# Kernel optimization log

Measured on AMD Instinct MI355X. Metric: run time of the kernel, lower is better.

Reference implementation:

```python
import jax, jax.numpy as jnp
import numpy as np

N, E, F, CUTOFF = 50000, 500000, 64, 5.0
EPS_CN, EPS_LN = 1e-8, 1e-5


def _xavier(k, shape):
    lim = float(np.sqrt(6.0 / (shape[0] + shape[1])))
    return jax.random.uniform(k, shape, jnp.float32, -lim, lim)


def setup_inputs() -> dict:
    key = jax.random.key(0)
    ks = jax.random.split(key, 20)
    vn = jax.random.normal(ks[5], (E, 3), jnp.float32)
    vn = vn / jnp.linalg.norm(vn, axis=-1, keepdims=True)  # unit direction vectors
    return {
        "node_s": jax.random.normal(ks[0], (N, 1, F), jnp.float32),
        "node_v": jax.random.normal(ks[1], (N, 3, F), jnp.float32),
        "edge_s": jax.random.normal(ks[2], (E, 1, F), jnp.float32),
        "edge_v": jax.random.normal(ks[3], (E, 3, F), jnp.float32),
        "dist": jax.random.uniform(ks[4], (E, 1), jnp.float32) * CUTOFF,
        "vctr_norm": vn,
        "src": jax.random.randint(ks[6], (E,), 0, N),
        "dst": jax.random.randint(ks[7], (E,), 0, N),
        "W_nn": _xavier(ks[8], (2 * F, F)), "b_nn": jnp.zeros((F,), jnp.float32),
        "W_ep": _xavier(ks[9], (F, F)), "b_ep": jnp.zeros((F,), jnp.float32),
        "W_g1": _xavier(ks[10], (F, F)), "b_g1": jnp.zeros((F,), jnp.float32),
        "W_g2": _xavier(ks[11], (F, F)), "b_g2": jnp.zeros((F,), jnp.float32),
        "W_ev": _xavier(ks[12], (F, 3 * F)), "b_ev": jnp.zeros((3 * F,), jnp.float32),
        "W_nvout": _xavier(ks[13], (F, 3 * F)),
        "W_nvc": _xavier(ks[14], (2 * F, F)), "b_nvc": jnp.zeros((F,), jnp.float32),
        "W_nvp": _xavier(ks[15], (F, 2 * F)),
        "W_nsp": _xavier(ks[16], (F, 2 * F)), "b_nsp": jnp.zeros((2 * F,), jnp.float32),
        "ln_gamma": jnp.ones((F,), jnp.float32), "ln_beta": jnp.zeros((F,), jnp.float32),
        "cn_scale": jnp.ones((F,), jnp.float32),
    }


def reference(node_s, node_v, edge_s, edge_v, dist, vctr_norm, src, dst,
              W_nn, b_nn, W_ep, b_ep, W_g1, b_g1, W_g2, b_g2, W_ev, b_ev,
              W_nvout, W_nvc, b_nvc, W_nvp, W_nsp, b_nsp, ln_gamma, ln_beta, cn_scale):
    n_nodes = node_s.shape[0]
    # cosine cutoff [E,1]
    c = 0.5 * (jnp.cos(jnp.pi * dist / CUTOFF) + 1.0) * (dist < CUTOFF).astype(dist.dtype)
    # ---- edge scalar update (gather src/dst, small MLPs) ----
    nn_in = jnp.concatenate([node_s[src], node_s[dst]], axis=-1)        # [E,1,2F]
    node_neighbors = nn_in @ W_nn + b_nn                                # [E,1,F]
    edge_message = node_neighbors * (edge_s @ W_ep + b_ep)              # [E,1,F]
    h = jax.nn.silu(edge_message @ W_g1 + b_g1)                         # GateMLP hidden
    es_upd = (h @ W_g2 + b_g2) * c[..., None]                           # [E,1,F]
    # ---- edge vector update ----
    vch = es_upd @ W_ev + b_ev                                          # [E,1,3F]
    nch, ech, rch = jnp.split(vch, 3, axis=-1)
    ev_upd = node_v[src] * nch + edge_v * ech + vctr_norm[..., None] * rch  # [E,3,F]
    ev_upd = ev_upd * c[..., None]
    # ---- scatter-mean to destination nodes ----
    deg = jax.ops.segment_sum(jnp.ones((src.shape[0],), node_s.dtype), dst, num_segments=n_nodes)
    denom = jnp.maximum(deg, 1.0)[:, None, None]
    n_ev = jax.ops.segment_sum(ev_upd, dst, num_segments=n_nodes) / denom  # [N,3,F]
    n_es = jax.ops.segment_sum(es_upd, dst, num_segments=n_nodes) / denom  # [N,1,F]
    # ---- node vector update ----
    nv_o1, nv_o2, nv_o3 = jnp.split(n_ev @ W_nvout, 3, axis=-1)          # each [N,3,F]
    v_in = jnp.concatenate([n_es, jnp.linalg.norm(nv_o3, axis=1, keepdims=True)], axis=-1)  # [N,1,2F]
    v_channel = v_in @ W_nvc + b_nvc                                     # [N,1,F]
    nv_upd = nv_o1 * v_channel + nv_o2                                   # [N,3,F]
    # ---- node scalar update ----
    nvp1, nvp2 = jnp.split(nv_upd @ W_nvp, 2, axis=-1)                   # [N,3,F] each
    ns1, ns2 = jnp.split(jax.nn.silu(n_es @ W_nsp + b_nsp), 2, axis=-1)  # [N,1,F] each
    nv_dot = jnp.sum(nvp1 * nvp2, axis=1, keepdims=True)                 # [N,1,F]
    ns_upd = nv_dot * ns1 + ns2                                          # [N,1,F]
    # ---- residuals + norms ----
    node_s_out = ns_upd + node_s
    node_v_out = nv_upd + node_v
    edge_s_out = es_upd + edge_s
    edge_v_out = ev_upd + edge_v
    # CoorsNorm: normalize over the 3D axis, learnable per-channel scale
    vnorm = jnp.linalg.norm(node_v_out, axis=1, keepdims=True)
    node_v_out = node_v_out / jnp.maximum(vnorm, EPS_CN) * cn_scale
    # LayerNorm over feature dim
    mu = jnp.mean(node_s_out, axis=-1, keepdims=True)
    var = jnp.var(node_s_out, axis=-1, keepdims=True)
    node_s_out = (node_s_out - mu) / jnp.sqrt(var + EPS_LN) * ln_gamma + ln_beta
    return node_s_out, node_v_out, edge_s_out, edge_v_out
```

## Files before the change

kernel.cpp:

```cpp
#include <hip/hip_runtime.h>
#include <hip/hip_bf16.h>
#include <math.h>

typedef __attribute__((ext_vector_type(8))) short bf16x8;
typedef __attribute__((ext_vector_type(4))) float f32x4;

#define MFMA16(a, b, c) __builtin_amdgcn_mfma_f32_16x16x32_bf16((a), (b), (c), 0, 0, 0)

__device__ __forceinline__ float silu_f(float x) { return x / (1.0f + expf(-x)); }

__device__ __forceinline__ unsigned short f2bf(float f) {
  union { __hip_bfloat16 h; unsigned short u; } c;
  c.h = __float2bfloat16(f);
  return c.u;
}
__device__ __forceinline__ unsigned pk2(float a, float b) {
  return (unsigned)f2bf(a) | ((unsigned)f2bf(b) << 16);
}

__device__ __forceinline__ bf16x8 ld_act(const unsigned short* buf, int strideB, int ks, int lane) {
  int row = lane & 15;
  int off = row * strideB + ks * 64 + ((lane >> 4) << 4);
  off ^= (row & 7) << 4;
  return *(const bf16x8*)((const char*)buf + off);
}

__device__ __forceinline__ bf16x8 ld_w(const unsigned short* Wt, int rowbase, int strideB, int ks, int lane) {
  return *(const bf16x8*)((const char*)Wt + (size_t)(rowbase + (lane & 15)) * strideB + ks * 64 + ((lane >> 4) << 4));
}

__global__ void wprep_kernel(const float* __restrict__ W, unsigned short* __restrict__ Wt,
                             int K, int Nn) {
  int idx = blockIdx.x * 256 + threadIdx.x;
  if (idx < K * Nn) {
    int n = idx / K, k = idx - n * K;
    Wt[idx] = f2bf(W[(size_t)k * Nn + n]);
  }
}

__global__ void hist_kernel(const int* __restrict__ dst, int* __restrict__ cnt, int E) {
  int i = blockIdx.x * blockDim.x + threadIdx.x;
  if (i < E) atomicAdd(&cnt[dst[i]], 1);
}

__global__ __launch_bounds__(1024) void scan_kernel(int* __restrict__ cnt,
                                                    int* __restrict__ rowstart, int N) {
  __shared__ int wsum[16];
  const int tid = threadIdx.x;
  const int wv = tid >> 6;
  int carry = 0;
  for (int base = 0; base < N; base += 1024) {
    int i = base + tid;
    int v = (i < N) ? cnt[i] : 0;
    int x = v;
    #pragma unroll
    for (int o = 1; o < 64; o <<= 1) {
      int y = __shfl_up(x, o);
      if ((tid & 63) >= o) x += y;
    }
    if ((tid & 63) == 63) wsum[wv] = x;
    __syncthreads();
    if (tid < 16) {
      int s = wsum[tid];
      #pragma unroll
      for (int o = 1; o < 16; o <<= 1) {
        int y = __shfl_up(s, o);
        if (tid >= o) s += y;
      }
      wsum[tid] = s;
    }
    __syncthreads();
    int woff = (wv > 0) ? wsum[wv - 1] : 0;
    if (i < N) {
      int excl = carry + woff + x - v;
      rowstart[i] = excl;
      cnt[i] = excl;
    }
    carry += wsum[15];
    __syncthreads();
  }
  if (tid == 0) rowstart[N] = carry;
}

__global__ void scatter_kernel(const int* __restrict__ dst, int* __restrict__ cursor,
                               int* __restrict__ elist, int E) {
  int i = blockIdx.x * blockDim.x + threadIdx.x;
  if (i < E) {
    int pos = atomicAdd(&cursor[dst[i]], 1);
    elist[pos] = i;
  }
}

__global__ __launch_bounds__(256) void edge_kernel(
    const float* __restrict__ node_s, const float* __restrict__ node_v,
    const float* __restrict__ edge_s, const float* __restrict__ edge_v,
    const float* __restrict__ dist,   const float* __restrict__ vctr,
    const int* __restrict__ src,      const int* __restrict__ dst,
    const unsigned short* __restrict__ wnn_t, const float* __restrict__ b_nn,
    const unsigned short* __restrict__ wep_t, const float* __restrict__ b_ep,
    const unsigned short* __restrict__ wg1_t, const float* __restrict__ b_g1,
    const unsigned short* __restrict__ wg2_t, const float* __restrict__ b_g2,
    const unsigned short* __restrict__ wev_t, const float* __restrict__ b_ev,
    float* __restrict__ es_out, float* __restrict__ ev_out,
    int E, int n_tiles)
{
  __shared__ __align__(16) unsigned short lds[4 * 3072];
  const int wid  = threadIdx.x >> 6;
  const int lane = threadIdx.x & 63;
  const int tile = blockIdx.x * 4 + wid;
  if (tile >= n_tiles) return;
  const int ebase = tile * 16;
  unsigned short* bufA = lds + wid * 3072;
  unsigned short* bufB = bufA + 2048;

  const int m  = lane & 15;
  const int nb = lane >> 4;

  {
    const int sm = lane >> 5;
    const int kk = lane & 31;
    #pragma unroll
    for (int p = 0; p < 8; ++p) {
      int le = p * 2 + sm;
      int e = ebase + le; if (e >= E) e = E - 1;
      int s = src[e], d = dst[e];
      float2 vs = *(const float2*)(node_s + (size_t)s * 64 + 2 * kk);
      float2 vd = *(const float2*)(node_s + (size_t)d * 64 + 2 * kk);
      float2 ve = *(const float2*)(edge_s + (size_t)e * 64 + 2 * kk);
      unsigned swz = (le & 7) << 4;
      *(unsigned*)((char*)bufA + ((le * 256 + kk * 4) ^ swz))       = pk2(vs.x, vs.y);
      *(unsigned*)((char*)bufA + ((le * 256 + 128 + kk * 4) ^ swz)) = pk2(vd.x, vd.y);
      *(unsigned*)((char*)bufB + ((le * 128 + kk * 4) ^ swz))       = pk2(ve.x, ve.y);
    }
  }
  __builtin_amdgcn_wave_barrier();

  const f32x4 z4 = {0.0f, 0.0f, 0.0f, 0.0f};

  bf16x8 a0 = ld_act(bufA, 256, 0, lane), a1 = ld_act(bufA, 256, 1, lane);
  bf16x8 a2 = ld_act(bufA, 256, 2, lane), a3 = ld_act(bufA, 256, 3, lane);
  f32x4 accN[4] = {z4, z4, z4, z4};
  #pragma unroll
  for (int nt = 0; nt < 4; ++nt) {
    accN[nt] = MFMA16(ld_w(wnn_t, nt * 16, 256, 0, lane), a0, accN[nt]);
    accN[nt] = MFMA16(ld_w(wnn_t, nt * 16, 256, 1, lane), a1, accN[nt]);
    accN[nt] = MFMA16(ld_w(wnn_t, nt * 16, 256, 2, lane), a2, accN[nt]);
    accN[nt] = MFMA16(ld_w(wnn_t, nt * 16, 256, 3, lane), a3, accN[nt]);
  }

  bf16x8 b0 = ld_act(bufB, 128, 0, lane), b1 = ld_act(bufB, 128, 1, lane);
  f32x4 accP[4] = {z4, z4, z4, z4};
  #pragma unroll
  for (int nt = 0; nt < 4; ++nt) {
    accP[nt] = MFMA16(ld_w(wep_t, nt * 16, 128, 0, lane), b0, accP[nt]);
    accP[nt] = MFMA16(ld_w(wep_t, nt * 16, 128, 1, lane), b1, accP[nt]);
  }

  const unsigned swzm = (m & 7) << 4;
  #pragma unroll
  for (int nt = 0; nt < 4; ++nt) {
    f32x4 bn = *(const f32x4*)(b_nn + nt * 16 + nb * 4);
    f32x4 bp = *(const f32x4*)(b_ep + nt * 16 + nb * 4);
    float e0 = (accN[nt].x + bn.x) * (accP[nt].x + bp.x);
    float e1 = (accN[nt].y + bn.y) * (accP[nt].y + bp.y);
    float e2 = (accN[nt].z + bn.z) * (accP[nt].z + bp.z);
    float e3 = (accN[nt].w + bn.w) * (accP[nt].w + bp.w);
    uint2 w2; w2.x = pk2(e0, e1); w2.y = pk2(e2, e3);
    *(uint2*)((char*)bufB + ((m * 128 + nt * 32 + nb * 8) ^ swzm)) = w2;
  }
  __builtin_amdgcn_wave_barrier();

  bf16x8 c0 = ld_act(bufB, 128, 0, lane), c1 = ld_act(bufB, 128, 1, lane);
  f32x4 accH[4] = {z4, z4, z4, z4};
  #pragma unroll
  for (int nt = 0; nt < 4; ++nt) {
    accH[nt] = MFMA16(ld_w(wg1_t, nt * 16, 128, 0, lane), c0, accH[nt]);
    accH[nt] = MFMA16(ld_w(wg1_t, nt * 16, 128, 1, lane), c1, accH[nt]);
  }
  #pragma unroll
  for (int nt = 0; nt < 4; ++nt) {
    f32x4 bg = *(const f32x4*)(b_g1 + nt * 16 + nb * 4);
    float h0 = silu_f(accH[nt].x + bg.x);
    float h1 = silu_f(accH[nt].y + bg.y);
    float h2 = silu_f(accH[nt].z + bg.z);
    float h3 = silu_f(accH[nt].w + bg.w);
    uint2 w2; w2.x = pk2(h0, h1); w2.y = pk2(h2, h3);
    *(uint2*)((char*)bufB + ((m * 128 + nt * 32 + nb * 8) ^ swzm)) = w2;
  }
  __builtin_amdgcn_wave_barrier();

  bf16x8 d0 = ld_act(bufB, 128, 0, lane), d1 = ld_act(bufB, 128, 1, lane);
  f32x4 accS[4] = {z4, z4, z4, z4};
  #pragma unroll
  for (int nt = 0; nt < 4; ++nt) {
    accS[nt] = MFMA16(ld_w(wg2_t, nt * 16, 128, 0, lane), d0, accS[nt]);
    accS[nt] = MFMA16(ld_w(wg2_t, nt * 16, 128, 1, lane), d1, accS[nt]);
  }
  const int e = ebase + m;
  float dd_ = dist[e];
  const float cc = (dd_ < 5.0f) ? 0.5f * (cosf(3.14159265358979f * dd_ * 0.2f) + 1.0f) : 0.0f;
  #pragma unroll
  for (int nt = 0; nt < 4; ++nt) {
    f32x4 bg = *(const f32x4*)(b_g2 + nt * 16 + nb * 4);
    accS[nt].x = (accS[nt].x + bg.x) * cc;
    accS[nt].y = (accS[nt].y + bg.y) * cc;
    accS[nt].z = (accS[nt].z + bg.z) * cc;
    accS[nt].w = (accS[nt].w + bg.w) * cc;
  }

  {
    const float* esrow = edge_s + (size_t)e * 64;
    float* eorow = es_out + (size_t)e * 64;
    #pragma unroll
    for (int nt = 0; nt < 4; ++nt) {
      float4 r = *(const float4*)(esrow + nt * 16 + nb * 4);
      float4 o;
      o.x = accS[nt].x + r.x; o.y = accS[nt].y + r.y;
      o.z = accS[nt].z + r.z; o.w = accS[nt].w + r.w;
      *(float4*)(eorow + nt * 16 + nb * 4) = o;
    }
  }

  #pragma unroll
  for (int nt = 0; nt < 4; ++nt) {
    uint2 w2;
    w2.x = pk2(accS[nt].x, accS[nt].y);
    w2.y = pk2(accS[nt].z, accS[nt].w);
    *(uint2*)((char*)bufB + ((m * 128 + nt * 32 + nb * 8) ^ swzm)) = w2;
  }
  __builtin_amdgcn_wave_barrier();

  bf16x8 g0 = ld_act(bufB, 128, 0, lane), g1f = ld_act(bufB, 128, 1, lane);
  f32x4 accV[12];
  #pragma unroll
  for (int i = 0; i < 12; ++i) accV[i] = z4;
  #pragma unroll
  for (int ch = 0; ch < 3; ++ch)
    #pragma unroll
    for (int nt = 0; nt < 4; ++nt) {
      accV[ch * 4 + nt] = MFMA16(ld_w(wev_t, ch * 64 + nt * 16, 128, 0, lane), g0,  accV[ch * 4 + nt]);
      accV[ch * 4 + nt] = MFMA16(ld_w(wev_t, ch * 64 + nt * 16, 128, 1, lane), g1f, accV[ch * 4 + nt]);
    }
  #pragma unroll
  for (int ch = 0; ch < 3; ++ch)
    #pragma unroll
    for (int nt = 0; nt < 4; ++nt) {
      f32x4 bv = *(const f32x4*)(b_ev + ch * 64 + nt * 16 + nb * 4);
      accV[ch * 4 + nt].x += bv.x; accV[ch * 4 + nt].y += bv.y;
      accV[ch * 4 + nt].z += bv.z; accV[ch * 4 + nt].w += bv.w;
    }

  {
    const int s = src[e];
    const float* nvb = node_v + (size_t)s * 192;
    const float* evb = edge_v + (size_t)e * 192;
    float* eob = ev_out + (size_t)e * 192;
    #pragma unroll
    for (int dd = 0; dd < 3; ++dd) {
      const float vn = vctr[e * 3 + dd];
      #pragma unroll
      for (int nt = 0; nt < 4; ++nt) {
        const int n0 = nt * 16 + nb * 4;
        float4 nv = *(const float4*)(nvb + dd * 64 + n0);
        float4 ev = *(const float4*)(evb + dd * 64 + n0);
        float4 o;
        o.x = (nv.x * accV[nt].x + ev.x * accV[4 + nt].x + vn * accV[8 + nt].x) * cc + ev.x;
        o.y = (nv.y * accV[nt].y + ev.y * accV[4 + nt].y + vn * accV[8 + nt].y) * cc + ev.y;
        o.z = (nv.z * accV[nt].z + ev.z * accV[4 + nt].z + vn * accV[8 + nt].z) * cc + ev.z;
        o.w = (nv.w * accV[nt].w + ev.w * accV[4 + nt].w + vn * accV[8 + nt].w) * cc + ev.w;
        *(float4*)(eob + dd * 64 + n0) = o;
      }
    }
  }
}

__device__ __forceinline__ void ld4(const float* p, float o[4]) {
  float4 v = *(const float4*)p;
  o[0] = v.x; o[1] = v.y; o[2] = v.z; o[3] = v.w;
}

__global__ __launch_bounds__(256) void node_kernel(
    const float* __restrict__ node_s, const float* __restrict__ node_v,
    const float* __restrict__ edge_s, const float* __restrict__ edge_v,
    const float* __restrict__ es_r,   const float* __restrict__ ev_r,
    const int* __restrict__ rowstart, const int* __restrict__ elist,
    const float* __restrict__ W_nvout,
    const float* __restrict__ W_nvc, const float* __restrict__ b_nvc,
    const float* __restrict__ W_nvp,
    const float* __restrict__ W_nsp, const float* __restrict__ b_nsp,
    const float* __restrict__ ln_g, const float* __restrict__ ln_b,
    const float* __restrict__ cn_s,
    float* __restrict__ ns_out, float* __restrict__ nv_out, int N)
{
  __shared__ __align__(16) float scm[4 * 8 * 68];
  const int wid = threadIdx.x >> 6, lane = threadIdx.x & 63;
  const int n = blockIdx.x * 4 + wid;
  if (n >= N) return;
  float* S = &scm[wid * 8 * 68];

  const int rs = rowstart[n], re = rowstart[n + 1];
  float nes = 0.0f, nev0 = 0.0f, nev1 = 0.0f, nev2 = 0.0f;
  for (int idx = rs; idx < re; ++idx) {
    int e = elist[idx];
    size_t b64 = (size_t)e * 64, b192 = (size_t)e * 192;
    nes  += es_r[b64 + lane]        - edge_s[b64 + lane];
    nev0 += ev_r[b192 + lane]       - edge_v[b192 + lane];
    nev1 += ev_r[b192 + 64 + lane]  - edge_v[b192 + 64 + lane];
    nev2 += ev_r[b192 + 128 + lane] - edge_v[b192 + 128 + lane];
  }
  const float inv = 1.0f / fmaxf((float)(re - rs), 1.0f);
  nes *= inv; nev0 *= inv; nev1 *= inv; nev2 *= inv;

  S[0 * 68 + lane] = nev0; S[1 * 68 + lane] = nev1;
  S[2 * 68 + lane] = nev2; S[3 * 68 + lane] = nes;
  __builtin_amdgcn_wave_barrier();

  float o1[3] = {}, o2[3] = {}, o3[3] = {};
  for (int k = 0; k < 64; k += 4) {
    float a0[4], a1[4], a2[4];
    ld4(S + 0 * 68 + k, a0); ld4(S + 1 * 68 + k, a1); ld4(S + 2 * 68 + k, a2);
    #pragma unroll
    for (int kk = 0; kk < 4; ++kk) {
      float w0 = W_nvout[(k + kk) * 192 + lane];
      float w1 = W_nvout[(k + kk) * 192 + 64 + lane];
      float w2 = W_nvout[(k + kk) * 192 + 128 + lane];
      o1[0] = fmaf(a0[kk], w0, o1[0]); o1[1] = fmaf(a1[kk], w0, o1[1]); o1[2] = fmaf(a2[kk], w0, o1[2]);
      o2[0] = fmaf(a0[kk], w1, o2[0]); o2[1] = fmaf(a1[kk], w1, o2[1]); o2[2] = fmaf(a2[kk], w1, o2[2]);
      o3[0] = fmaf(a0[kk], w2, o3[0]); o3[1] = fmaf(a1[kk], w2, o3[1]); o3[2] = fmaf(a2[kk], w2, o3[2]);
    }
  }
  float nrm = sqrtf(o3[0] * o3[0] + o3[1] * o3[1] + o3[2] * o3[2]);
  S[4 * 68 + lane] = nrm;
  __builtin_amdgcn_wave_barrier();

  float vch = 0.0f;
  for (int k = 0; k < 64; k += 4) {
    float a[4], b[4];
    ld4(S + 3 * 68 + k, a); ld4(S + 4 * 68 + k, b);
    #pragma unroll
    for (int kk = 0; kk < 4; ++kk) {
      vch = fmaf(a[kk], W_nvc[(k + kk) * 64 + lane], vch);
      vch = fmaf(b[kk], W_nvc[(64 + k + kk) * 64 + lane], vch);
    }
  }
  vch += b_nvc[lane];

  float nvu[3];
  #pragma unroll
  for (int dd = 0; dd < 3; ++dd) {
    nvu[dd] = o1[dd] * vch + o2[dd];
    S[(5 + dd) * 68 + lane] = nvu[dd];
  }
  __builtin_amdgcn_wave_barrier();

  float p1[3] = {}, p2[3] = {};
  for (int k = 0; k < 64; k += 4) {
    float a0[4], a1[4], a2[4];
    ld4(S + 5 * 68 + k, a0); ld4(S + 6 * 68 + k, a1); ld4(S + 7 * 68 + k, a2);
    #pragma unroll
    for (int kk = 0; kk < 4; ++kk) {
      float w1 = W_nvp[(k + kk) * 128 + lane];
      float w2 = W_nvp[(k + kk) * 128 + 64 + lane];
      p1[0] = fmaf(a0[kk], w1, p1[0]); p1[1] = fmaf(a1[kk], w1, p1[1]); p1[2] = fmaf(a2[kk], w1, p1[2]);
      p2[0] = fmaf(a0[kk], w2, p2[0]); p2[1] = fmaf(a1[kk], w2, p2[1]); p2[2] = fmaf(a2[kk], w2, p2[2]);
    }
  }

  float s1a = 0.0f, s2a = 0.0f;
  for (int k = 0; k < 64; k += 4) {
    float a[4];
    ld4(S + 3 * 68 + k, a);
    #pragma unroll
    for (int kk = 0; kk < 4; ++kk) {
      s1a = fmaf(a[kk], W_nsp[(k + kk) * 128 + lane], s1a);
      s2a = fmaf(a[kk], W_nsp[(k + kk) * 128 + 64 + lane], s2a);
    }
  }
  float s1 = silu_f(s1a + b_nsp[lane]);
  float s2 = silu_f(s2a + b_nsp[64 + lane]);

  float nvdot = p1[0] * p2[0] + p1[1] * p2[1] + p1[2] * p2[2];
  float nsu = nvdot * s1 + s2;

  float xs = nsu + node_s[n * 64 + lane];
  float sum = xs, sumsq = xs * xs;
  #pragma unroll
  for (int o = 32; o; o >>= 1) {
    sum += __shfl_xor(sum, o);
    sumsq += __shfl_xor(sumsq, o);
  }
  float mu = sum * (1.0f / 64.0f);
  float var = sumsq * (1.0f / 64.0f) - mu * mu;
  ns_out[n * 64 + lane] = (xs - mu) * rsqrtf(var + 1e-5f) * ln_g[lane] + ln_b[lane];

  float vv[3];
  #pragma unroll
  for (int dd = 0; dd < 3; ++dd) vv[dd] = nvu[dd] + node_v[n * 192 + dd * 64 + lane];
  float vn2 = sqrtf(vv[0] * vv[0] + vv[1] * vv[1] + vv[2] * vv[2]);
  float scale = cn_s[lane] / fmaxf(vn2, 1e-8f);
  #pragma unroll
  for (int dd = 0; dd < 3; ++dd)
    nv_out[n * 192 + dd * 64 + lane] = vv[dd] * scale;
}

extern "C" void kernel_launch(void* const* d_in, const int* in_sizes, int n_in,
                              void* d_out, int out_size, void* d_ws, size_t ws_size,
                              hipStream_t stream) {
  const float* node_s = (const float*)d_in[0];
  const float* node_v = (const float*)d_in[1];
  const float* edge_s = (const float*)d_in[2];
  const float* edge_v = (const float*)d_in[3];
  const float* dist   = (const float*)d_in[4];
  const float* vctr   = (const float*)d_in[5];
  const int*   src    = (const int*)d_in[6];
  const int*   dst    = (const int*)d_in[7];
  const float* W_nn = (const float*)d_in[8];  const float* b_nn = (const float*)d_in[9];
  const float* W_ep = (const float*)d_in[10]; const float* b_ep = (const float*)d_in[11];
  const float* W_g1 = (const float*)d_in[12]; const float* b_g1 = (const float*)d_in[13];
  const float* W_g2 = (const float*)d_in[14]; const float* b_g2 = (const float*)d_in[15];
  const float* W_ev = (const float*)d_in[16]; const float* b_ev = (const float*)d_in[17];
  const float* W_nvout = (const float*)d_in[18];
  const float* W_nvc = (const float*)d_in[19]; const float* b_nvc = (const float*)d_in[20];
  const float* W_nvp = (const float*)d_in[21];
  const float* W_nsp = (const float*)d_in[22]; const float* b_nsp = (const float*)d_in[23];
  const float* ln_g = (const float*)d_in[24]; const float* ln_b = (const float*)d_in[25];
  const float* cn_s = (const float*)d_in[26];

  const int N = in_sizes[0] / 64;
  const int E = in_sizes[2] / 64;

  float* out    = (float*)d_out;
  float* ns_out = out;
  float* nv_out = out + (size_t)N * 64;
  float* es_out = out + (size_t)N * 256;
  float* ev_out = out + (size_t)N * 256 + (size_t)E * 64;

  int* cnt      = (int*)d_ws;
  int* rowstart = cnt + N;
  int* elist    = rowstart + N + 1;
  unsigned short* wnn_t = (unsigned short*)(elist + E);
  unsigned short* wep_t = wnn_t + 64 * 128;
  unsigned short* wg1_t = wep_t + 64 * 64;
  unsigned short* wg2_t = wg1_t + 64 * 64;
  unsigned short* wev_t = wg2_t + 64 * 64;

  hipMemsetAsync(cnt, 0, (size_t)N * sizeof(int), stream);
  hist_kernel<<<(E + 255) / 256, 256, 0, stream>>>(dst, cnt, E);
  scan_kernel<<<1, 1024, 0, stream>>>(cnt, rowstart, N);
  scatter_kernel<<<(E + 255) / 256, 256, 0, stream>>>(dst, cnt, elist, E);

  wprep_kernel<<<(64 * 128 + 255) / 256, 256, 0, stream>>>(W_nn, wnn_t, 128, 64);
  wprep_kernel<<<(64 * 64 + 255) / 256, 256, 0, stream>>>(W_ep, wep_t, 64, 64);
  wprep_kernel<<<(64 * 64 + 255) / 256, 256, 0, stream>>>(W_g1, wg1_t, 64, 64);
  wprep_kernel<<<(64 * 64 + 255) / 256, 256, 0, stream>>>(W_g2, wg2_t, 64, 64);
  wprep_kernel<<<(192 * 64 + 255) / 256, 256, 0, stream>>>(W_ev, wev_t, 64, 192);

  int n_tiles = (E + 15) / 16;
  edge_kernel<<<(n_tiles + 3) / 4, 256, 0, stream>>>(
      node_s, node_v, edge_s, edge_v, dist, vctr, src, dst,
      wnn_t, b_nn, wep_t, b_ep, wg1_t, b_g1, wg2_t, b_g2, wev_t, b_ev,
      es_out, ev_out, E, n_tiles);

  node_kernel<<<(N + 3) / 4, 256, 0, stream>>>(
      node_s, node_v, edge_s, edge_v, es_out, ev_out, rowstart, elist,
      W_nvout, W_nvc, b_nvc, W_nvp, W_nsp, b_nsp,
      ln_g, ln_b, cn_s, ns_out, nv_out, N);
}
```

Before: 1.096 ms.

## Write bf16 edge updates in dst-sorted order for contiguous node aggregation

The edge kernel now also stores the pre-residual edge updates as bf16 into a workspace buffer, placed at each edge's position in the dst-sorted edge list (recorded by the scatter pass). The node kernel then streams those contiguous bf16 rows instead of gathering fp32 outputs and inputs through elist and subtracting the residual. This removes the random gather traffic and halves the bytes read in aggregation, at the cost of extra bf16 writes and reduced aggregation precision. The edge kernel is also restructured to fuse MFMA stages per tile, load edge_s directly into registers, cut LDS use, and add an occupancy hint to launch bounds.

```diff
diff --git a/kernel.cpp b/kernel.cpp
--- a/kernel.cpp
+++ b/kernel.cpp
@@ -16,6 +16,11 @@
 }
 __device__ __forceinline__ unsigned pk2(float a, float b) {
   return (unsigned)f2bf(a) | ((unsigned)f2bf(b) << 16);
+}
+__device__ __forceinline__ float bfu(unsigned short u) {
+  union { unsigned u32; float f; } c;
+  c.u32 = (unsigned)u << 16;
+  return c.f;
 }
 
 __device__ __forceinline__ bf16x8 ld_act(const unsigned short* buf, int strideB, int ks, int lane) {
@@ -83,35 +88,37 @@
 }
 
 __global__ void scatter_kernel(const int* __restrict__ dst, int* __restrict__ cursor,
-                               int* __restrict__ elist, int E) {
+                               int* __restrict__ elist, int* __restrict__ epos, int E) {
   int i = blockIdx.x * blockDim.x + threadIdx.x;
   if (i < E) {
     int pos = atomicAdd(&cursor[dst[i]], 1);
     elist[pos] = i;
-  }
-}
-
-__global__ __launch_bounds__(256) void edge_kernel(
+    epos[i] = pos;
+  }
+}
+
+__global__ __launch_bounds__(256, 8) void edge_kernel(
     const float* __restrict__ node_s, const float* __restrict__ node_v,
     const float* __restrict__ edge_s, const float* __restrict__ edge_v,
     const float* __restrict__ dist,   const float* __restrict__ vctr,
     const int* __restrict__ src,      const int* __restrict__ dst,
+    const int* __restrict__ epos,
     const unsigned short* __restrict__ wnn_t, const float* __restrict__ b_nn,
     const unsigned short* __restrict__ wep_t, const float* __restrict__ b_ep,
     const unsigned short* __restrict__ wg1_t, const float* __restrict__ b_g1,
     const unsigned short* __restrict__ wg2_t, const float* __restrict__ b_g2,
     const unsigned short* __restrict__ wev_t, const float* __restrict__ b_ev,
     float* __restrict__ es_out, float* __restrict__ ev_out,
-    int E, int n_tiles)
+    unsigned short* __restrict__ raw_es, unsigned short* __restrict__ raw_ev,
+    int use_raw, int E, int n_tiles)
 {
-  __shared__ __align__(16) unsigned short lds[4 * 3072];
+  __shared__ __align__(16) unsigned short lds[4 * 2048];
   const int wid  = threadIdx.x >> 6;
   const int lane = threadIdx.x & 63;
   const int tile = blockIdx.x * 4 + wid;
   if (tile >= n_tiles) return;
   const int ebase = tile * 16;
-  unsigned short* bufA = lds + wid * 3072;
-  unsigned short* bufB = bufA + 2048;
+  unsigned short* bufA = lds + wid * 2048;
 
   const int m  = lane & 15;
   const int nb = lane >> 4;
@@ -126,148 +133,139 @@
       int s = src[e], d = dst[e];
       float2 vs = *(const float2*)(node_s + (size_t)s * 64 + 2 * kk);
       float2 vd = *(const float2*)(node_s + (size_t)d * 64 + 2 * kk);
-      float2 ve = *(const float2*)(edge_s + (size_t)e * 64 + 2 * kk);
       unsigned swz = (le & 7) << 4;
       *(unsigned*)((char*)bufA + ((le * 256 + kk * 4) ^ swz))       = pk2(vs.x, vs.y);
       *(unsigned*)((char*)bufA + ((le * 256 + 128 + kk * 4) ^ swz)) = pk2(vd.x, vd.y);
-      *(unsigned*)((char*)bufB + ((le * 128 + kk * 4) ^ swz))       = pk2(ve.x, ve.y);
-    }
-  }
-  __builtin_amdgcn_wave_barrier();
+    }
+  }
+  __builtin_amdgcn_wave_barrier();
+
+  const int e = (ebase + m < E) ? ebase + m : E - 1;
+  const float dd_ = dist[e];
+  const float cc = (dd_ < 5.0f) ? 0.5f * (cosf(3.14159265358979f * dd_ * 0.2f) + 1.0f) : 0.0f;
+  const int s_nd = src[e];
+  int pos = 0;
+  if (use_raw) pos = epos[e];
 
   const f32x4 z4 = {0.0f, 0.0f, 0.0f, 0.0f};
+  const unsigned swzm = (m & 7) << 4;
 
   bf16x8 a0 = ld_act(bufA, 256, 0, lane), a1 = ld_act(bufA, 256, 1, lane);
   bf16x8 a2 = ld_act(bufA, 256, 2, lane), a3 = ld_act(bufA, 256, 3, lane);
-  f32x4 accN[4] = {z4, z4, z4, z4};
+
+  const float* esrow = edge_s + (size_t)e * 64;
+  bf16x8 b0, b1;
+  {
+    const int k8 = (lane >> 4) << 3;
+    float4 p0 = *(const float4*)(esrow + k8);
+    float4 p1 = *(const float4*)(esrow + k8 + 4);
+    float4 q0 = *(const float4*)(esrow + 32 + k8);
+    float4 q1 = *(const float4*)(esrow + 32 + k8 + 4);
+    union { bf16x8 v; uint4 u; } cb;
+    cb.u.x = pk2(p0.x, p0.y); cb.u.y = pk2(p0.z, p0.w);
+    cb.u.z = pk2(p1.x, p1.y); cb.u.w = pk2(p1.z, p1.w);
+    b0 = cb.v;
+    cb.u.x = pk2(q0.x, q0.y); cb.u.y = pk2(q0.z, q0.w);
+    cb.u.z = pk2(q1.x, q1.y); cb.u.w = pk2(q1.z, q1.w);
+    b1 = cb.v;
+  }
+  __builtin_amdgcn_wave_barrier();
+
   #pragma unroll
   for (int nt = 0; nt < 4; ++nt) {
-    accN[nt] = MFMA16(ld_w(wnn_t, nt * 16, 256, 0, lane), a0, accN[nt]);
-    accN[nt] = MFMA16(ld_w(wnn_t, nt * 16, 256, 1, lane), a1, accN[nt]);
-    accN[nt] = MFMA16(ld_w(wnn_t, nt * 16, 256, 2, lane), a2, accN[nt]);
-    accN[nt] = MFMA16(ld_w(wnn_t, nt * 16, 256, 3, lane), a3, accN[nt]);
-  }
-
-  bf16x8 b0 = ld_act(bufB, 128, 0, lane), b1 = ld_act(bufB, 128, 1, lane);
-  f32x4 accP[4] = {z4, z4, z4, z4};
-  #pragma unroll
-  for (int nt = 0; nt < 4; ++nt) {
-    accP[nt] = MFMA16(ld_w(wep_t, nt * 16, 128, 0, lane), b0, accP[nt]);
-    accP[nt] = MFMA16(ld_w(wep_t, nt * 16, 128, 1, lane), b1, accP[nt]);
-  }
-
-  const unsigned swzm = (m & 7) << 4;
-  #pragma unroll
-  for (int nt = 0; nt < 4; ++nt) {
+    f32x4 aN = z4, aP = z4;
+    aN = MFMA16(ld_w(wnn_t, nt * 16, 256, 0, lane), a0, aN);
+    aN = MFMA16(ld_w(wnn_t, nt * 16, 256, 1, lane), a1, aN);
+    aN = MFMA16(ld_w(wnn_t, nt * 16, 256, 2, lane), a2, aN);
+    aN = MFMA16(ld_w(wnn_t, nt * 16, 256, 3, lane), a3, aN);
+    aP = MFMA16(ld_w(wep_t, nt * 16, 128, 0, lane), b0, aP);
+    aP = MFMA16(ld_w(wep_t, nt * 16, 128, 1, lane), b1, aP);
     f32x4 bn = *(const f32x4*)(b_nn + nt * 16 + nb * 4);
     f32x4 bp = *(const f32x4*)(b_ep + nt * 16 + nb * 4);
-    float e0 = (accN[nt].x + bn.x) * (accP[nt].x + bp.x);
-    float e1 = (accN[nt].y + bn.y) * (accP[nt].y + bp.y);
-    float e2 = (accN[nt].z + bn.z) * (accP[nt].z + bp.z);
-    float e3 = (accN[nt].w + bn.w) * (accP[nt].w + bp.w);
+    float e0 = (aN.x + bn.x) * (aP.x + bp.x);
+    float e1 = (aN.y + bn.y) * (aP.y + bp.y);
+    float e2 = (aN.z + bn.z) * (aP.z + bp.z);
+    float e3 = (aN.w + bn.w) * (aP.w + bp.w);
     uint2 w2; w2.x = pk2(e0, e1); w2.y = pk2(e2, e3);
-    *(uint2*)((char*)bufB + ((m * 128 + nt * 32 + nb * 8) ^ swzm)) = w2;
-  }
-  __builtin_amdgcn_wave_barrier();
-
-  bf16x8 c0 = ld_act(bufB, 128, 0, lane), c1 = ld_act(bufB, 128, 1, lane);
-  f32x4 accH[4] = {z4, z4, z4, z4};
+    *(uint2*)((char*)bufA + ((m * 128 + nt * 32 + nb * 8) ^ swzm)) = w2;
+  }
+  __builtin_amdgcn_wave_barrier();
+
+  bf16x8 c0 = ld_act(bufA, 128, 0, lane), c1 = ld_act(bufA, 128, 1, lane);
+  __builtin_amdgcn_wave_barrier();
   #pragma unroll
   for (int nt = 0; nt < 4; ++nt) {
-    accH[nt] = MFMA16(ld_w(wg1_t, nt * 16, 128, 0, lane), c0, accH[nt]);
-    accH[nt] = MFMA16(ld_w(wg1_t, nt * 16, 128, 1, lane), c1, accH[nt]);
-  }
+    f32x4 aH = z4;
+    aH = MFMA16(ld_w(wg1_t, nt * 16, 128, 0, lane), c0, aH);
+    aH = MFMA16(ld_w(wg1_t, nt * 16, 128, 1, lane), c1, aH);
+    f32x4 bg = *(const f32x4*)(b_g1 + nt * 16 + nb * 4);
+    uint2 w2;
+    w2.x = pk2(silu_f(aH.x + bg.x), silu_f(aH.y + bg.y));
+    w2.y = pk2(silu_f(aH.z + bg.z), silu_f(aH.w + bg.w));
+    *(uint2*)((char*)bufA + ((m * 128 + nt * 32 + nb * 8) ^ swzm)) = w2;
+  }
+  __builtin_amdgcn_wave_barrier();
+
+  bf16x8 d0 = ld_act(bufA, 128, 0, lane), d1 = ld_act(bufA, 128, 1, lane);
+  __builtin_amdgcn_wave_barrier();
+  float* eorow = es_out + (size_t)e * 64;
   #pragma unroll
   for (int nt = 0; nt < 4; ++nt) {
-    f32x4 bg = *(const f32x4*)(b_g1 + nt * 16 + nb * 4);
-    float h0 = silu_f(accH[nt].x + bg.x);
-    float h1 = silu_f(accH[nt].y + bg.y);
-    float h2 = silu_f(accH[nt].z + bg.z);
-    float h3 = silu_f(accH[nt].w + bg.w);
-    uint2 w2; w2.x = pk2(h0, h1); w2.y = pk2(h2, h3);
-    *(uint2*)((char*)bufB + ((m * 128 + nt * 32 + nb * 8) ^ swzm)) = w2;
-  }
-  __builtin_amdgcn_wave_barrier();
-
-  bf16x8 d0 = ld_act(bufB, 128, 0, lane), d1 = ld_act(bufB, 128, 1, lane);
-  f32x4 accS[4] = {z4, z4, z4, z4};
+    f32x4 aS = z4;
+    aS = MFMA16(ld_w(wg2_t, nt * 16, 128, 0, lane), d0, aS);
+    aS = MFMA16(ld_w(wg2_t, nt * 16, 128, 1, lane), d1, aS);
+    f32x4 bg = *(const f32x4*)(b_g2 + nt * 16 + nb * 4);
+    float u0 = (aS.x + bg.x) * cc, u1 = (aS.y + bg.y) * cc;
+    float u2 = (aS.z + bg.z) * cc, u3 = (aS.w + bg.w) * cc;
+    const int n0 = nt * 16 + nb * 4;
+    uint2 w2; w2.x = pk2(u0, u1); w2.y = pk2(u2, u3);
+    *(uint2*)((char*)bufA + ((m * 128 + nt * 32 + nb * 8) ^ swzm)) = w2;
+    if (use_raw) *(uint2*)(raw_es + (size_t)pos * 64 + n0) = w2;
+    if (ebase + m < E) {
+      float4 r = *(const float4*)(esrow + n0);
+      float4 o; o.x = u0 + r.x; o.y = u1 + r.y; o.z = u2 + r.z; o.w = u3 + r.w;
+      *(float4*)(eorow + n0) = o;
+    }
+  }
+  __builtin_amdgcn_wave_barrier();
+
+  bf16x8 g0 = ld_act(bufA, 128, 0, lane), g1f = ld_act(bufA, 128, 1, lane);
+  const float* nvb = node_v + (size_t)s_nd * 192;
+  const float* evb = edge_v + (size_t)e * 192;
+  float* eob = ev_out + (size_t)e * 192;
+  float vnn0 = vctr[e * 3], vnn1 = vctr[e * 3 + 1], vnn2 = vctr[e * 3 + 2];
+  const bool live = (ebase + m < E);
   #pragma unroll
   for (int nt = 0; nt < 4; ++nt) {
-    accS[nt] = MFMA16(ld_w(wg2_t, nt * 16, 128, 0, lane), d0, accS[nt]);
-    accS[nt] = MFMA16(ld_w(wg2_t, nt * 16, 128, 1, lane), d1, accS[nt]);
-  }
-  const int e = ebase + m;
-  float dd_ = dist[e];
-  const float cc = (dd_ < 5.0f) ? 0.5f * (cosf(3.14159265358979f * dd_ * 0.2f) + 1.0f) : 0.0f;
-  #pragma unroll
-  for (int nt = 0; nt < 4; ++nt) {
-    f32x4 bg = *(const f32x4*)(b_g2 + nt * 16 + nb * 4);
-    accS[nt].x = (accS[nt].x + bg.x) * cc;
-    accS[nt].y = (accS[nt].y + bg.y) * cc;
-    accS[nt].z = (accS[nt].z + bg.z) * cc;
-    accS[nt].w = (accS[nt].w + bg.w) * cc;
-  }
-
-  {
-    const float* esrow = edge_s + (size_t)e * 64;
-    float* eorow = es_out + (size_t)e * 64;
-    #pragma unroll
-    for (int nt = 0; nt < 4; ++nt) {
-      float4 r = *(const float4*)(esrow + nt * 16 + nb * 4);
-      float4 o;
-      o.x = accS[nt].x + r.x; o.y = accS[nt].y + r.y;
-      o.z = accS[nt].z + r.z; o.w = accS[nt].w + r.w;
-      *(float4*)(eorow + nt * 16 + nb * 4) = o;
-    }
-  }
-
-  #pragma unroll
-  for (int nt = 0; nt < 4; ++nt) {
-    uint2 w2;
-    w2.x = pk2(accS[nt].x, accS[nt].y);
-    w2.y = pk2(accS[nt].z, accS[nt].w);
-    *(uint2*)((char*)bufB + ((m * 128 + nt * 32 + nb * 8) ^ swzm)) = w2;
-  }
-  __builtin_amdgcn_wave_barrier();
-
-  bf16x8 g0 = ld_act(bufB, 128, 0, lane), g1f = ld_act(bufB, 128, 1, lane);
-  f32x4 accV[12];
-  #pragma unroll
-  for (int i = 0; i < 12; ++i) accV[i] = z4;
-  #pragma unroll
-  for (int ch = 0; ch < 3; ++ch)
-    #pragma unroll
-    for (int nt = 0; nt < 4; ++nt) {
-      accV[ch * 4 + nt] = MFMA16(ld_w(wev_t, ch * 64 + nt * 16, 128, 0, lane), g0,  accV[ch * 4 + nt]);
-      accV[ch * 4 + nt] = MFMA16(ld_w(wev_t, ch * 64 + nt * 16, 128, 1, lane), g1f, accV[ch * 4 + nt]);
-    }
-  #pragma unroll
-  for (int ch = 0; ch < 3; ++ch)
-    #pragma unroll
-    for (int nt = 0; nt < 4; ++nt) {
-      f32x4 bv = *(const f32x4*)(b_ev + ch * 64 + nt * 16 + nb * 4);
-      accV[ch * 4 + nt].x += bv.x; accV[ch * 4 + nt].y += bv.y;
-      accV[ch * 4 + nt].z += bv.z; accV[ch * 4 + nt].w += bv.w;
-    }
-
-  {
-    const int s = src[e];
-    const float* nvb = node_v + (size_t)s * 192;
-    const float* evb = edge_v + (size_t)e * 192;
-    float* eob = ev_out + (size_t)e * 192;
+    f32x4 aN = z4, aE = z4, aR = z4;
+    aN = MFMA16(ld_w(wev_t,        nt * 16, 128, 0, lane), g0,  aN);
+    aN = MFMA16(ld_w(wev_t,        nt * 16, 128, 1, lane), g1f, aN);
+    aE = MFMA16(ld_w(wev_t,  64 + nt * 16, 128, 0, lane), g0,  aE);
+    aE = MFMA16(ld_w(wev_t,  64 + nt * 16, 128, 1, lane), g1f, aE);
+    aR = MFMA16(ld_w(wev_t, 128 + nt * 16, 128, 0, lane), g0,  aR);
+    aR = MFMA16(ld_w(wev_t, 128 + nt * 16, 128, 1, lane), g1f, aR);
+    const int n0 = nt * 16 + nb * 4;
+    f32x4 bv0 = *(const f32x4*)(b_ev + n0);
+    f32x4 bv1 = *(const f32x4*)(b_ev + 64 + n0);
+    f32x4 bv2 = *(const f32x4*)(b_ev + 128 + n0);
+    aN.x += bv0.x; aN.y += bv0.y; aN.z += bv0.z; aN.w += bv0.w;
+    aE.x += bv1.x; aE.y += bv1.y; aE.z += bv1.z; aE.w += bv1.w;
+    aR.x += bv2.x; aR.y += bv2.y; aR.z += bv2.z; aR.w += bv2.w;
     #pragma unroll
     for (int dd = 0; dd < 3; ++dd) {
-      const float vn = vctr[e * 3 + dd];
-      #pragma unroll
-      for (int nt = 0; nt < 4; ++nt) {
-        const int n0 = nt * 16 + nb * 4;
-        float4 nv = *(const float4*)(nvb + dd * 64 + n0);
-        float4 ev = *(const float4*)(evb + dd * 64 + n0);
-        float4 o;
-        o.x = (nv.x * accV[nt].x + ev.x * accV[4 + nt].x + vn * accV[8 + nt].x) * cc + ev.x;
-        o.y = (nv.y * accV[nt].y + ev.y * accV[4 + nt].y + vn * accV[8 + nt].y) * cc + ev.y;
-        o.z = (nv.z * accV[nt].z + ev.z * accV[4 + nt].z + vn * accV[8 + nt].z) * cc + ev.z;
-        o.w = (nv.w * accV[nt].w + ev.w * accV[4 + nt].w + vn * accV[8 + nt].w) * cc + ev.w;
+      const float vn = (dd == 0) ? vnn0 : (dd == 1) ? vnn1 : vnn2;
+      float4 nv = *(const float4*)(nvb + dd * 64 + n0);
+      float4 ev = *(const float4*)(evb + dd * 64 + n0);
+      float eu0 = (nv.x * aN.x + ev.x * aE.x + vn * aR.x) * cc;
+      float eu1 = (nv.y * aN.y + ev.y * aE.y + vn * aR.y) * cc;
+      float eu2 = (nv.z * aN.z + ev.z * aE.z + vn * aR.z) * cc;
+      float eu3 = (nv.w * aN.w + ev.w * aE.w + vn * aR.w) * cc;
+      if (use_raw) {
+        uint2 r; r.x = pk2(eu0, eu1); r.y = pk2(eu2, eu3);
+        *(uint2*)(raw_ev + (size_t)pos * 192 + dd * 64 + n0) = r;
+      }
+      if (live) {
+        float4 o; o.x = eu0 + ev.x; o.y = eu1 + ev.y; o.z = eu2 + ev.z; o.w = eu3 + ev.w;
         *(float4*)(eob + dd * 64 + n0) = o;
       }
     }
@@ -283,7 +281,8 @@
     const float* __restrict__ node_s, const float* __restrict__ node_v,
     const float* __restrict__ edge_s, const float* __restrict__ edge_v,
     const float* __restrict__ es_r,   const float* __restrict__ ev_r,
-    const int* __restrict__ rowstart, const int* __restrict__ elist,
+    const unsigned short* __restrict__ raw_es, const unsigned short* __restrict__ raw_ev,
+    const int* __restrict__ rowstart, const int* __restrict__ elist, int use_raw,
     const float* __restrict__ W_nvout,
     const float* __restrict__ W_nvc, const float* __restrict__ b_nvc,
     const float* __restrict__ W_nvp,
@@ -300,13 +299,33 @@
 
   const int rs = rowstart[n], re = rowstart[n + 1];
   float nes = 0.0f, nev0 = 0.0f, nev1 = 0.0f, nev2 = 0.0f;
-  for (int idx = rs; idx < re; ++idx) {
-    int e = elist[idx];
-    size_t b64 = (size_t)e * 64, b192 = (size_t)e * 192;
-    nes  += es_r[b64 + lane]        - edge_s[b64 + lane];
-    nev0 += ev_r[b192 + lane]       - edge_v[b192 + lane];
-    nev1 += ev_r[b192 + 64 + lane]  - edge_v[b192 + 64 + lane];
-    nev2 += ev_r[b192 + 128 + lane] - edge_v[b192 + 128 + lane];
+  if (use_raw) {
+    const unsigned short* pe = raw_es + (size_t)rs * 64 + lane;
+    const unsigned short* pv = raw_ev + (size_t)rs * 192 + lane;
+    int idx = rs;
+    for (; idx + 1 < re; idx += 2) {
+      unsigned short e0 = pe[0], e1 = pe[64];
+      unsigned short v00 = pv[0], v01 = pv[64], v02 = pv[128];
+      unsigned short v10 = pv[192], v11 = pv[256], v12 = pv[320];
+      nes  += bfu(e0) + bfu(e1);
+      nev0 += bfu(v00) + bfu(v10);
+      nev1 += bfu(v01) + bfu(v11);
+      nev2 += bfu(v02) + bfu(v12);
+      pe += 128; pv += 384;
+    }
+    if (idx < re) {
+      nes  += bfu(pe[0]);
+      nev0 += bfu(pv[0]); nev1 += bfu(pv[64]); nev2 += bfu(pv[128]);
+    }
+  } else {
+    for (int idx = rs; idx < re; ++idx) {
+      int e = elist[idx];
+      size_t b64 = (size_t)e * 64, b192 = (size_t)e * 192;
+      nes  += es_r[b64 + lane]        - edge_s[b64 + lane];
+      nev0 += ev_r[b192 + lane]       - edge_v[b192 + lane];
+      nev1 += ev_r[b192 + 64 + lane]  - edge_v[b192 + 64 + lane];
+      nev2 += ev_r[b192 + 128 + lane] - edge_v[b192 + 128 + lane];
+    }
   }
   const float inv = 1.0f / fmaxf((float)(re - rs), 1.0f);
   nes *= inv; nev0 *= inv; nev1 *= inv; nev2 *= inv;
@@ -437,17 +456,24 @@
 
   int* cnt      = (int*)d_ws;
   int* rowstart = cnt + N;
-  int* elist    = rowstart + N + 1;
+  int* epos     = rowstart + N + 1;
+  int* elist    = epos + E;
   unsigned short* wnn_t = (unsigned short*)(elist + E);
   unsigned short* wep_t = wnn_t + 64 * 128;
   unsigned short* wg1_t = wep_t + 64 * 64;
   unsigned short* wg2_t = wg1_t + 64 * 64;
   unsigned short* wev_t = wg2_t + 64 * 64;
+  size_t wend = (size_t)((char*)(wev_t + 192 * 64) - (char*)d_ws);
+  size_t rawofs = (wend + 255) & ~(size_t)255;
+  unsigned short* raw_es = (unsigned short*)((char*)d_ws + rawofs);
+  unsigned short* raw_ev = raw_es + (size_t)E * 64;
+  size_t need = rawofs + (size_t)E * 256 * sizeof(unsigned short);
+  int use_raw = (ws_size >= need) ? 1 : 0;
 
   hipMemsetAsync(cnt, 0, (size_t)N * sizeof(int), stream);
   hist_kernel<<<(E + 255) / 256, 256, 0, stream>>>(dst, cnt, E);
   scan_kernel<<<1, 1024, 0, stream>>>(cnt, rowstart, N);
-  scatter_kernel<<<(E + 255) / 256, 256, 0, stream>>>(dst, cnt, elist, E);
+  scatter_kernel<<<(E + 255) / 256, 256, 0, stream>>>(dst, cnt, elist, epos, E);
 
   wprep_kernel<<<(64 * 128 + 255) / 256, 256, 0, stream>>>(W_nn, wnn_t, 128, 64);
   wprep_kernel<<<(64 * 64 + 255) / 256, 256, 0, stream>>>(W_ep, wep_t, 64, 64);
@@ -457,12 +483,13 @@
 
   int n_tiles = (E + 15) / 16;
   edge_kernel<<<(n_tiles + 3) / 4, 256, 0, stream>>>(
-      node_s, node_v, edge_s, edge_v, dist, vctr, src, dst,
+      node_s, node_v, edge_s, edge_v, dist, vctr, src, dst, epos,
       wnn_t, b_nn, wep_t, b_ep, wg1_t, b_g1, wg2_t, b_g2, wev_t, b_ev,
-      es_out, ev_out, E, n_tiles);
+      es_out, ev_out, raw_es, raw_ev, use_raw, E, n_tiles);
 
   node_kernel<<<(N + 3) / 4, 256, 0, stream>>>(
-      node_s, node_v, edge_s, edge_v, es_out, ev_out, rowstart, elist,
+      node_s, node_v, edge_s, edge_v, es_out, ev_out, raw_es, raw_ev,
+      rowstart, elist, use_raw,
       W_nvout, W_nvc, b_nvc, W_nvp, W_nsp, b_nsp,
       ln_g, ln_b, cn_s, ns_out, nv_out, N);
 }
```

New measurement: 1.201 ms. 9.5% more time.
